# Optimization experiments

Measured on AMD Instinct MI355X. Metric: run time of the kernel, lower is better.

Reference implementation:

```python
import jax, jax.numpy as jnp
import numpy as np

N = 50000
E = 400000


def _cheb_norm(edge_index, dtype):
    # PyG ChebConv norm (normalization='sym', lambda_max=2.0):
    # remove self loops, L_hat = -D^{-1/2} A D^{-1/2} on off-diagonal edges.
    src, dst = edge_index[0], edge_index[1]
    mask = (src != dst).astype(dtype)
    deg = jax.ops.segment_sum(mask, src, num_segments=N)
    dinv = jnp.where(deg > 0, jax.lax.rsqrt(jnp.where(deg > 0, deg, 1.0)), 0.0)
    w = -dinv[src] * dinv[dst] * mask  # [E]
    return src, dst, w


def _cheb_conv(x, src, dst, w, W0, W1, b):
    # out = T0(x) W0 + T1(x) W1 + b, T0 = x, T1 = L_hat x
    tx1 = jax.ops.segment_sum(w[:, None] * x[src], dst, num_segments=N)
    return x @ W0 + tx1 @ W1 + b


def setup_inputs() -> dict:
    key = jax.random.key(0)
    ks = jax.random.split(key, 12)
    s = 0.05
    inp = {
        "x": jax.random.normal(ks[0], (N, 128), dtype=jnp.float32),
        "edge_index": jax.random.randint(ks[1], (2, E), 0, N, dtype=jnp.int64),
        "W1_0": jax.random.normal(ks[2], (128, 256), dtype=jnp.float32) * s,
        "W1_1": jax.random.normal(ks[3], (128, 256), dtype=jnp.float32) * s,
        "b1": jnp.zeros((256,), dtype=jnp.float32),
        "W2_0": jax.random.normal(ks[4], (256, 256), dtype=jnp.float32) * s,
        "W2_1": jax.random.normal(ks[5], (256, 256), dtype=jnp.float32) * s,
        "b2": jnp.zeros((256,), dtype=jnp.float32),
        "W3_0": jax.random.normal(ks[6], (256, 256), dtype=jnp.float32) * s,
        "W3_1": jax.random.normal(ks[7], (256, 256), dtype=jnp.float32) * s,
        "b3": jnp.zeros((256,), dtype=jnp.float32),
    }
    return inp


def reference(x, edge_index, W1_0, W1_1, b1, W2_0, W2_1, b2, W3_0, W3_1, b3):
    # Eval mode: F.dropout with training=False is identity, so dropout is omitted.
    src, dst, w = _cheb_norm(edge_index, x.dtype)
    h = jax.nn.relu(_cheb_conv(x, src, dst, w, W1_0, W1_1, b1))
    h = jax.nn.relu(_cheb_conv(h, src, dst, w, W2_0, W2_1, b2))
    h = _cheb_conv(h, src, dst, w, W3_0, W3_1, b3)
    return h
```

## Files before the change

kernel.cpp:

```cpp
#include <hip/hip_runtime.h>
#include <hip/hip_bf16.h>


typedef __attribute__((ext_vector_type(8))) short bf16x8;
typedef __attribute__((ext_vector_type(4))) float f32x4;

__device__ __forceinline__ float bf2f(unsigned int lo16) {
    unsigned int t = lo16 << 16;
    return __builtin_bit_cast(float, t);
}
__device__ __forceinline__ unsigned short f2bf(float f) {
    unsigned int u = __builtin_bit_cast(unsigned int, f);
    unsigned int r = (u + 0x7fffu + ((u >> 16) & 1u)) >> 16;
    return (unsigned short)r;
}

struct PrepParams {
    const int* src;
    const int* dst;
    float* deg;
    int* cnt;
    int E;
    const float* x;
    unsigned short* xb;
    int gE;
    int gC;
    const float* W[6];
    unsigned short* WT[6];
    int K[6];
};

__global__ __launch_bounds__(256) void prep_kernel(PrepParams p) {
    __shared__ float t[32][33];
    int b = blockIdx.x;
    int tid = threadIdx.x;
    if (b < p.gE) {
        int e = b * 256 + tid;
        if (e < p.E) {
            int s = p.src[e], d = p.dst[e];
            if (s != d) atomicAdd(&p.deg[s], 1.0f);
            atomicAdd(&p.cnt[d], 1);
        }
        return;
    }
    b -= p.gE;
    if (b < p.gC) {
        long long i = (long long)b * 256 + tid;
        float4 v = reinterpret_cast<const float4*>(p.x)[i];
        ushort4 o;
        o.x = f2bf(v.x); o.y = f2bf(v.y); o.z = f2bf(v.z); o.w = f2bf(v.w);
        reinterpret_cast<ushort4*>(p.xb)[i] = o;
        return;
    }
    b -= p.gC;
    int m = b >> 6;
    int rem = b & 63;
    int K = p.K[m];
    int kb = (rem & 7) * 32, nb = (rem >> 3) * 32;
    if (kb >= K) return;
    const float* W = p.W[m];
    unsigned short* WT = p.WT[m];
    int lx = tid & 31, ly = tid >> 5;
    #pragma unroll
    for (int i = 0; i < 32; i += 8)
        t[ly + i][lx] = W[(size_t)(kb + ly + i) * 256 + nb + lx];
    __syncthreads();
    #pragma unroll
    for (int i = 0; i < 32; i += 8)
        WT[(size_t)(nb + ly + i) * K + kb + lx] = f2bf(t[lx][ly + i]);
}

__global__ __launch_bounds__(256) void scan_partial_dinv(const int* __restrict__ cnt,
                                                         int* __restrict__ part,
                                                         float* __restrict__ deg, int N) {
    __shared__ int lds[256];
    int tid = threadIdx.x;
    int base = blockIdx.x * 1024 + tid * 4;
    int s = 0;
    #pragma unroll
    for (int i = 0; i < 4; ++i) {
        if (base + i < N) {
            s += cnt[base + i];
            float d = deg[base + i];
            deg[base + i] = (d > 0.0f) ? rsqrtf(d) : 0.0f;
        }
    }
    lds[tid] = s;
    __syncthreads();
    for (int off = 128; off > 0; off >>= 1) {
        if (tid < off) lds[tid] += lds[tid + off];
        __syncthreads();
    }
    if (tid == 0) part[blockIdx.x] = lds[0];
}

__global__ __launch_bounds__(64) void scan_small(int* __restrict__ part, int NB,
                                                 int* __restrict__ rowptr, int N) {
    int lane = threadIdx.x;
    int v = (lane < NB) ? part[lane] : 0;
    int inc = v;
    #pragma unroll
    for (int off = 1; off < 64; off <<= 1) {
        int t = __shfl_up(inc, off, 64);
        if (lane >= off) inc += t;
    }
    if (lane < NB) part[lane] = inc - v;
    if (lane == 63) rowptr[N] = inc;
}

__global__ __launch_bounds__(256) void scan_chunk(const int* __restrict__ cnt,
                                                  const int* __restrict__ part,
                                                  int* __restrict__ rowptr, int N) {
    __shared__ int lds[256];
    int tid = threadIdx.x;
    int base = blockIdx.x * 1024 + tid * 4;
    int c[4];
    #pragma unroll
    for (int i = 0; i < 4; ++i) c[i] = (base + i < N) ? cnt[base + i] : 0;
    int ts = c[0] + c[1] + c[2] + c[3];
    lds[tid] = ts;
    __syncthreads();
    for (int off = 1; off < 256; off <<= 1) {
        int v = (tid >= off) ? lds[tid - off] : 0;
        __syncthreads();
        lds[tid] += v;
        __syncthreads();
    }
    int o = part[blockIdx.x] + lds[tid] - ts;
    #pragma unroll
    for (int i = 0; i < 4; ++i) {
        if (base + i < N) rowptr[base + i] = o;
        o += c[i];
    }
}

__global__ __launch_bounds__(256) void fill_kernel(const int* __restrict__ src,
                                                   const int* __restrict__ dst,
                                                   const float* __restrict__ dinv,
                                                   const int* __restrict__ rowptr,
                                                   int* __restrict__ cnt2,
                                                   int* __restrict__ esrc,
                                                   float* __restrict__ ew, int E) {
    int e = blockIdx.x * blockDim.x + threadIdx.x;
    if (e < E) {
        int s = src[e], d = dst[e];
        int pos = rowptr[d] + atomicAdd(&cnt2[d], 1);
        esrc[pos] = s;
        ew[pos] = (s != d) ? (-dinv[s] * dinv[d]) : 0.0f;
    }
}

template <int V> struct RowT;
template <> struct RowT<4> { using T = uint2; };
template <> struct RowT<8> { using T = uint4; };

__device__ __forceinline__ void fma_row(float* acc, uint2 u, float wv) {
    acc[0] += wv * bf2f(u.x & 0xffffu);
    acc[1] += wv * bf2f(u.x >> 16);
    acc[2] += wv * bf2f(u.y & 0xffffu);
    acc[3] += wv * bf2f(u.y >> 16);
}
__device__ __forceinline__ void fma_row(float* acc, uint4 u, float wv) {
    acc[0] += wv * bf2f(u.x & 0xffffu);
    acc[1] += wv * bf2f(u.x >> 16);
    acc[2] += wv * bf2f(u.y & 0xffffu);
    acc[3] += wv * bf2f(u.y >> 16);
    acc[4] += wv * bf2f(u.z & 0xffffu);
    acc[5] += wv * bf2f(u.z >> 16);
    acc[6] += wv * bf2f(u.w & 0xffffu);
    acc[7] += wv * bf2f(u.w >> 16);
}
__device__ __forceinline__ void pack_out(unsigned short* q, const float* acc, uint2*) {
    uint2 o;
    o.x = (unsigned int)f2bf(acc[0]) | ((unsigned int)f2bf(acc[1]) << 16);
    o.y = (unsigned int)f2bf(acc[2]) | ((unsigned int)f2bf(acc[3]) << 16);
    *reinterpret_cast<uint2*>(q) = o;
}
__device__ __forceinline__ void pack_out(unsigned short* q, const float* acc, uint4*) {
    uint4 o;
    o.x = (unsigned int)f2bf(acc[0]) | ((unsigned int)f2bf(acc[1]) << 16);
    o.y = (unsigned int)f2bf(acc[2]) | ((unsigned int)f2bf(acc[3]) << 16);
    o.z = (unsigned int)f2bf(acc[4]) | ((unsigned int)f2bf(acc[5]) << 16);
    o.w = (unsigned int)f2bf(acc[6]) | ((unsigned int)f2bf(acc[7]) << 16);
    *reinterpret_cast<uint4*>(q) = o;
}

template <int F>
__global__ __launch_bounds__(256) void gather_bf16(const int* __restrict__ rowptr,
                                                   const int* __restrict__ esrc,
                                                   const float* __restrict__ ew,
                                                   const unsigned short* __restrict__ xb,
                                                   unsigned short* __restrict__ txb,
                                                   int N) {
    constexpr int V = F / 32;
    using T = typename RowT<V>::T;
    int half = threadIdx.x >> 5;
    int lane = threadIdx.x & 31;
    int n = blockIdx.x * 8 + half;
    if (n >= N) return;
    int beg = rowptr[n], end = rowptr[n + 1];
    float acc[V] = {};

    int k = beg;
    for (; k + 4 <= end; k += 4) {
        int s0 = esrc[k], s1 = esrc[k + 1], s2 = esrc[k + 2], s3 = esrc[k + 3];
        float w0 = ew[k], w1 = ew[k + 1], w2 = ew[k + 2], w3 = ew[k + 3];
        T r0 = *reinterpret_cast<const T*>(&xb[(size_t)s0 * F + lane * V]);
        T r1 = *reinterpret_cast<const T*>(&xb[(size_t)s1 * F + lane * V]);
        T r2 = *reinterpret_cast<const T*>(&xb[(size_t)s2 * F + lane * V]);
        T r3 = *reinterpret_cast<const T*>(&xb[(size_t)s3 * F + lane * V]);
        fma_row(acc, r0, w0);
        fma_row(acc, r1, w1);
        fma_row(acc, r2, w2);
        fma_row(acc, r3, w3);
    }
    for (; k < end; ++k) {
        int s = esrc[k];
        float wv = ew[k];
        T r = *reinterpret_cast<const T*>(&xb[(size_t)s * F + lane * V]);
        fma_row(acc, r, wv);
    }

    pack_out(&txb[(size_t)n * F + lane * V], acc, (T*)nullptr);
}

template <int K, bool RELU, typename OutT>
__global__ __launch_bounds__(256, 3) void gemm_mfma(const unsigned short* __restrict__ Xb,
                                                    const unsigned short* __restrict__ Tb,
                                                    const unsigned short* __restrict__ W0T,
                                                    const unsigned short* __restrict__ W1T,
                                                    const float* __restrict__ bias,
                                                    OutT* __restrict__ out, int M) {
    __shared__ unsigned short As[64 * 64];
    __shared__ unsigned short Bs[256 * 64];

    const int tid = threadIdx.x;
    const int wave = tid >> 6;
    const int lane = tid & 63;
    const int l15 = lane & 15;
    const int quad = lane >> 4;
    const int row0 = blockIdx.x * 64;
    const int swz = ((lane & 7) ^ ((lane >> 3) & 7)) * 8;

    f32x4 acc[4][4];
    #pragma unroll
    for (int i = 0; i < 4; ++i)
        #pragma unroll
        for (int j = 0; j < 4; ++j) acc[i][j] = (f32x4){0.f, 0.f, 0.f, 0.f};

    typedef const __attribute__((address_space(1))) void gvoid;
    typedef __attribute__((address_space(3))) void lvoid;

    #pragma unroll
    for (int pass = 0; pass < 2; ++pass) {
        const unsigned short* Amat = pass ? Tb : Xb;
        const unsigned short* Wmat = pass ? W1T : W0T;
        for (int k0 = 0; k0 < K; k0 += 64) {
            if (pass != 0 || k0 != 0) __syncthreads();
            #pragma unroll
            for (int r = 0; r < 2; ++r) {
                int grow = row0 + r * 32 + wave * 8 + (lane >> 3);
                if (grow > M - 1) grow = M - 1;
                const unsigned short* gp = &Amat[(size_t)grow * K + k0 + swz];
                __builtin_amdgcn_global_load_lds((gvoid*)gp,
                    (lvoid*)&As[(r * 32 + wave * 8) * 64], 16, 0, 0);
            }
            #pragma unroll
            for (int r = 0; r < 8; ++r) {
                int brow = r * 32 + wave * 8 + (lane >> 3);
                const unsigned short* gp = &Wmat[(size_t)brow * K + k0 + swz];
                __builtin_amdgcn_global_load_lds((gvoid*)gp,
                    (lvoid*)&Bs[(r * 32 + wave * 8) * 64], 16, 0, 0);
            }
            __syncthreads();

            #pragma unroll
            for (int kf = 0; kf < 2; ++kf) {
                const int col = (((kf * 4 + quad) ^ (l15 & 7)) * 8);
                bf16x8 a[4], b[4];
                #pragma unroll
                for (int mt = 0; mt < 4; ++mt)
                    a[mt] = *reinterpret_cast<const bf16x8*>(&As[(mt * 16 + l15) * 64 + col]);
                #pragma unroll
                for (int nt = 0; nt < 4; ++nt)
                    b[nt] = *reinterpret_cast<const bf16x8*>(
                        &Bs[(wave * 64 + nt * 16 + l15) * 64 + col]);
                #pragma unroll
                for (int mt = 0; mt < 4; ++mt)
                    #pragma unroll
                    for (int nt = 0; nt < 4; ++nt)
                        acc[mt][nt] = __builtin_amdgcn_mfma_f32_16x16x32_bf16(
                            a[mt], b[nt], acc[mt][nt], 0, 0, 0);
            }
        }
    }

    #pragma unroll
    for (int mt = 0; mt < 4; ++mt) {
        #pragma unroll
        for (int r = 0; r < 4; ++r) {
            int m = row0 + mt * 16 + quad * 4 + r;
            if (m >= M) continue;
            #pragma unroll
            for (int nt = 0; nt < 4; ++nt) {
                int n = wave * 64 + nt * 16 + l15;
                float v = acc[mt][nt][r] + bias[n];
                if (RELU) v = fmaxf(v, 0.0f);
                if constexpr (sizeof(OutT) == 2)
                    out[(size_t)m * 256 + n] = (OutT)f2bf(v);
                else
                    out[(size_t)m * 256 + n] = (OutT)v;
            }
        }
    }
}

static inline size_t align_up(size_t v, size_t a) { return (v + a - 1) / a * a; }

extern "C" void kernel_launch(void* const* d_in, const int* in_sizes, int n_in,
                              void* d_out, int out_size, void* d_ws, size_t ws_size,
                              hipStream_t stream) {
    const float* x    = (const float*)d_in[0];
    const int*   ei   = (const int*)d_in[1];
    const float* W1_0 = (const float*)d_in[2];
    const float* W1_1 = (const float*)d_in[3];
    const float* b1   = (const float*)d_in[4];
    const float* W2_0 = (const float*)d_in[5];
    const float* W2_1 = (const float*)d_in[6];
    const float* b2   = (const float*)d_in[7];
    const float* W3_0 = (const float*)d_in[8];
    const float* W3_1 = (const float*)d_in[9];
    const float* b3   = (const float*)d_in[10];
    float* out = (float*)d_out;

    const int N = in_sizes[0] / 128;
    const int E = in_sizes[1] / 2;
    const int* src = ei;
    const int* dst = ei + E;

    typedef unsigned short u16;
    char* ws = (char*)d_ws;
    size_t off = 0;
    float* dinv   = (float*)(ws + off); off = align_up(off + (size_t)N * 4, 256);
    int*   cnt    = (int*)  (ws + off); off = align_up(off + (size_t)N * 4, 256);
    int*   cnt2   = (int*)  (ws + off); off = align_up(off + (size_t)N * 4, 256);
    size_t zero_end = off;
    int*   rowptr = (int*)  (ws + off); off = align_up(off + (size_t)(N + 1) * 4, 256);
    int*   part   = (int*)  (ws + off); off = align_up(off + 256 * 4, 256);
    int*   esrc   = (int*)  (ws + off); off = align_up(off + (size_t)E * 4, 256);
    float* ew     = (float*)(ws + off); off = align_up(off + (size_t)E * 4, 256);
    u16*   xb     = (u16*)  (ws + off); off = align_up(off + (size_t)N * 128 * 2, 256);
    u16*   txb    = (u16*)  (ws + off); off = align_up(off + (size_t)N * 256 * 2, 256);
    u16*   h1b    = (u16*)  (ws + off); off = align_up(off + (size_t)N * 256 * 2, 256);
    u16*   h2b    = (u16*)  (ws + off); off = align_up(off + (size_t)N * 256 * 2, 256);
    u16*   W10T   = (u16*)  (ws + off); off = align_up(off + (size_t)256 * 128 * 2, 256);
    u16*   W11T   = (u16*)  (ws + off); off = align_up(off + (size_t)256 * 128 * 2, 256);
    u16*   W20T   = (u16*)  (ws + off); off = align_up(off + (size_t)256 * 256 * 2, 256);
    u16*   W21T   = (u16*)  (ws + off); off = align_up(off + (size_t)256 * 256 * 2, 256);
    u16*   W30T   = (u16*)  (ws + off); off = align_up(off + (size_t)256 * 256 * 2, 256);
    u16*   W31T   = (u16*)  (ws + off); off = align_up(off + (size_t)256 * 256 * 2, 256);
    (void)ws_size;

    const int TB = 256;
    const int gE = (E + TB - 1) / TB;
    const int gC = (int)(((long long)N * 128 / 4) / 256);
    const int NB = (N + 1023) / 1024;

    hipMemsetAsync(dinv, 0, zero_end, stream);

    {
        PrepParams p;
        p.src = src; p.dst = dst; p.deg = dinv; p.cnt = cnt; p.E = E;
        p.x = x; p.xb = xb; p.gE = gE; p.gC = gC;
        p.W[0] = W1_0; p.WT[0] = W10T; p.K[0] = 128;
        p.W[1] = W1_1; p.WT[1] = W11T; p.K[1] = 128;
        p.W[2] = W2_0; p.WT[2] = W20T; p.K[2] = 256;
        p.W[3] = W2_1; p.WT[3] = W21T; p.K[3] = 256;
        p.W[4] = W3_0; p.WT[4] = W30T; p.K[4] = 256;
        p.W[5] = W3_1; p.WT[5] = W31T; p.K[5] = 256;
        prep_kernel<<<gE + gC + 384, TB, 0, stream>>>(p);
    }

    scan_partial_dinv<<<NB, 256, 0, stream>>>(cnt, part, dinv, N);
    scan_small<<<1, 64, 0, stream>>>(part, NB, rowptr, N);
    scan_chunk<<<NB, 256, 0, stream>>>(cnt, part, rowptr, N);
    fill_kernel<<<(E + TB - 1) / TB, TB, 0, stream>>>(src, dst, dinv, rowptr, cnt2,
                                                      esrc, ew, E);

    dim3 gemmGrid((N + 63) / 64);
    dim3 gatherGrid((N + 7) / 8);

    gather_bf16<128><<<gatherGrid, TB, 0, stream>>>(rowptr, esrc, ew, xb, txb, N);
    gemm_mfma<128, true, u16><<<gemmGrid, TB, 0, stream>>>(xb, txb, W10T, W11T, b1, h1b, N);

    gather_bf16<256><<<gatherGrid, TB, 0, stream>>>(rowptr, esrc, ew, h1b, txb, N);
    gemm_mfma<256, true, u16><<<gemmGrid, TB, 0, stream>>>(h1b, txb, W20T, W21T, b2, h2b, N);

    gather_bf16<256><<<gatherGrid, TB, 0, stream>>>(rowptr, esrc, ew, h2b, txb, N);
    gemm_mfma<256, false, float><<<gemmGrid, TB, 0, stream>>>(h2b, txb, W30T, W31T, b3, out, N);
}
```

Before: 329.0 us.

## Build CSR with LDS-chunked histograms and shrink GEMM row tile to 32

Replaces the global-atomic degree/count and fill passes with per-chunk, per-range shared-memory histograms. Their counts are reduced and prefix-scanned into per-chunk bases, so the fill is deterministic and each edge takes an LDS atomic rank instead of a global atomic. The memset disappears because every histogram cell is written. Separately, the GEMM tile drops from 64 to 32 rows with occupancy hint 4, which doubles the grid but reuses the B tile less and reloads it twice as often.

```diff
diff --git a/kernel.cpp b/kernel.cpp
--- a/kernel.cpp
+++ b/kernel.cpp
@@ -4,6 +4,10 @@
 
 typedef __attribute__((ext_vector_type(8))) short bf16x8;
 typedef __attribute__((ext_vector_type(4))) float f32x4;
+
+#define NCH 16
+#define RBITS 13
+#define RBINS 8192
 
 __device__ __forceinline__ float bf2f(unsigned int lo16) {
     unsigned int t = lo16 << 16;
@@ -16,34 +20,18 @@
 }
 
 struct PrepParams {
-    const int* src;
-    const int* dst;
-    float* deg;
-    int* cnt;
-    int E;
     const float* x;
     unsigned short* xb;
-    int gE;
     int gC;
     const float* W[6];
     unsigned short* WT[6];
     int K[6];
 };
 
-__global__ __launch_bounds__(256) void prep_kernel(PrepParams p) {
+__global__ __launch_bounds__(256) void prep2_kernel(PrepParams p) {
     __shared__ float t[32][33];
     int b = blockIdx.x;
     int tid = threadIdx.x;
-    if (b < p.gE) {
-        int e = b * 256 + tid;
-        if (e < p.E) {
-            int s = p.src[e], d = p.dst[e];
-            if (s != d) atomicAdd(&p.deg[s], 1.0f);
-            atomicAdd(&p.cnt[d], 1);
-        }
-        return;
-    }
-    b -= p.gE;
     if (b < p.gC) {
         long long i = (long long)b * 256 + tid;
         float4 v = reinterpret_cast<const float4*>(p.x)[i];
@@ -70,19 +58,61 @@
         WT[(size_t)(nb + ly + i) * K + kb + lx] = f2bf(t[lx][ly + i]);
 }
 
-__global__ __launch_bounds__(256) void scan_partial_dinv(const int* __restrict__ cnt,
-                                                         int* __restrict__ part,
-                                                         float* __restrict__ deg, int N) {
+__global__ __launch_bounds__(256) void hist_kernel(const int* __restrict__ src,
+                                                   const int* __restrict__ dst,
+                                                   int* __restrict__ H,
+                                                   int* __restrict__ H2,
+                                                   int E, int NR, int NPAD) {
+    __shared__ int h[RBINS];
+    int tid = threadIdx.x;
+    int b = blockIdx.x;
+    int srcpass = (b >= NCH * NR);
+    if (srcpass) b -= NCH * NR;
+    int c = b / NR, r = b % NR;
+    int r0 = r << RBITS;
+    for (int i = tid; i < RBINS; i += 256) h[i] = 0;
+    __syncthreads();
+    int EC = (E + NCH - 1) / NCH;
+    int e0 = c * EC, e1 = min(e0 + EC, E);
+    if (!srcpass) {
+        for (int e = e0 + tid; e < e1; e += 256) {
+            int d = dst[e] - r0;
+            if ((unsigned)d < RBINS) atomicAdd(&h[d], 1);
+        }
+    } else {
+        for (int e = e0 + tid; e < e1; e += 256) {
+            int s = src[e];
+            int d = s - r0;
+            if ((unsigned)d < RBINS && s != dst[e]) atomicAdd(&h[d], 1);
+        }
+    }
+    __syncthreads();
+    int* out = (srcpass ? H2 : H) + (size_t)c * NPAD + r0;
+    for (int i = tid; i < RBINS; i += 256) out[i] = h[i];
+}
+
+__global__ __launch_bounds__(256) void reduce_scan_partial(const int* __restrict__ H,
+                                                           const int* __restrict__ H2,
+                                                           int* __restrict__ cnt,
+                                                           float* __restrict__ dinv,
+                                                           int* __restrict__ part,
+                                                           int N, int NPAD) {
     __shared__ int lds[256];
     int tid = threadIdx.x;
     int base = blockIdx.x * 1024 + tid * 4;
     int s = 0;
     #pragma unroll
     for (int i = 0; i < 4; ++i) {
-        if (base + i < N) {
-            s += cnt[base + i];
-            float d = deg[base + i];
-            deg[base + i] = (d > 0.0f) ? rsqrtf(d) : 0.0f;
+        int d = base + i;
+        if (d < N) {
+            int cn = 0, dg = 0;
+            for (int c = 0; c < NCH; ++c) {
+                cn += H[(size_t)c * NPAD + d];
+                dg += H2[(size_t)c * NPAD + d];
+            }
+            cnt[d] = cn;
+            dinv[d] = (dg > 0) ? rsqrtf((float)dg) : 0.0f;
+            s += cn;
         }
     }
     lds[tid] = s;
@@ -108,16 +138,19 @@
     if (lane == 63) rowptr[N] = inc;
 }
 
-__global__ __launch_bounds__(256) void scan_chunk(const int* __restrict__ cnt,
-                                                  const int* __restrict__ part,
-                                                  int* __restrict__ rowptr, int N) {
+__global__ __launch_bounds__(256) void scan_chunk_base(const int* __restrict__ cnt,
+                                                       const int* __restrict__ part,
+                                                       const int* __restrict__ H,
+                                                       int* __restrict__ rowptr,
+                                                       int* __restrict__ HS,
+                                                       int N, int NPAD) {
     __shared__ int lds[256];
     int tid = threadIdx.x;
     int base = blockIdx.x * 1024 + tid * 4;
-    int c[4];
-    #pragma unroll
-    for (int i = 0; i < 4; ++i) c[i] = (base + i < N) ? cnt[base + i] : 0;
-    int ts = c[0] + c[1] + c[2] + c[3];
+    int c4[4];
+    #pragma unroll
+    for (int i = 0; i < 4; ++i) c4[i] = (base + i < N) ? cnt[base + i] : 0;
+    int ts = c4[0] + c4[1] + c4[2] + c4[3];
     lds[tid] = ts;
     __syncthreads();
     for (int off = 1; off < 256; off <<= 1) {
@@ -129,24 +162,45 @@
     int o = part[blockIdx.x] + lds[tid] - ts;
     #pragma unroll
     for (int i = 0; i < 4; ++i) {
-        if (base + i < N) rowptr[base + i] = o;
-        o += c[i];
+        int d = base + i;
+        if (d < N) {
+            rowptr[d] = o;
+            int run = o;
+            for (int c = 0; c < NCH; ++c) {
+                HS[(size_t)c * NPAD + d] = run;
+                run += H[(size_t)c * NPAD + d];
+            }
+            o = run;
+        }
     }
 }
 
 __global__ __launch_bounds__(256) void fill_kernel(const int* __restrict__ src,
                                                    const int* __restrict__ dst,
                                                    const float* __restrict__ dinv,
-                                                   const int* __restrict__ rowptr,
-                                                   int* __restrict__ cnt2,
+                                                   const int* __restrict__ HS,
                                                    int* __restrict__ esrc,
-                                                   float* __restrict__ ew, int E) {
-    int e = blockIdx.x * blockDim.x + threadIdx.x;
-    if (e < E) {
-        int s = src[e], d = dst[e];
-        int pos = rowptr[d] + atomicAdd(&cnt2[d], 1);
-        esrc[pos] = s;
-        ew[pos] = (s != d) ? (-dinv[s] * dinv[d]) : 0.0f;
+                                                   float* __restrict__ ew,
+                                                   int E, int NR, int NPAD) {
+    __shared__ int h[RBINS];
+    int tid = threadIdx.x;
+    int b = blockIdx.x;
+    int c = b / NR, r = b % NR;
+    int r0 = r << RBITS;
+    for (int i = tid; i < RBINS; i += 256) h[i] = 0;
+    __syncthreads();
+    int EC = (E + NCH - 1) / NCH;
+    int e0 = c * EC, e1 = min(e0 + EC, E);
+    for (int e = e0 + tid; e < e1; e += 256) {
+        int d = dst[e];
+        int dl = d - r0;
+        if ((unsigned)dl < RBINS) {
+            int s = src[e];
+            int rank = atomicAdd(&h[dl], 1);
+            int pos = HS[(size_t)c * NPAD + d] + rank;
+            esrc[pos] = s;
+            ew[pos] = (s != d) ? (-dinv[s] * dinv[d]) : 0.0f;
+        }
     }
 }
 
@@ -225,13 +279,13 @@
 }
 
 template <int K, bool RELU, typename OutT>
-__global__ __launch_bounds__(256, 3) void gemm_mfma(const unsigned short* __restrict__ Xb,
+__global__ __launch_bounds__(256, 4) void gemm_mfma(const unsigned short* __restrict__ Xb,
                                                     const unsigned short* __restrict__ Tb,
                                                     const unsigned short* __restrict__ W0T,
                                                     const unsigned short* __restrict__ W1T,
                                                     const float* __restrict__ bias,
                                                     OutT* __restrict__ out, int M) {
-    __shared__ unsigned short As[64 * 64];
+    __shared__ unsigned short As[32 * 64];
     __shared__ unsigned short Bs[256 * 64];
 
     const int tid = threadIdx.x;
@@ -239,12 +293,12 @@
     const int lane = tid & 63;
     const int l15 = lane & 15;
     const int quad = lane >> 4;
-    const int row0 = blockIdx.x * 64;
+    const int row0 = blockIdx.x * 32;
     const int swz = ((lane & 7) ^ ((lane >> 3) & 7)) * 8;
 
-    f32x4 acc[4][4];
-    #pragma unroll
-    for (int i = 0; i < 4; ++i)
+    f32x4 acc[2][4];
+    #pragma unroll
+    for (int i = 0; i < 2; ++i)
         #pragma unroll
         for (int j = 0; j < 4; ++j) acc[i][j] = (f32x4){0.f, 0.f, 0.f, 0.f};
 
@@ -257,13 +311,12 @@
         const unsigned short* Wmat = pass ? W1T : W0T;
         for (int k0 = 0; k0 < K; k0 += 64) {
             if (pass != 0 || k0 != 0) __syncthreads();
-            #pragma unroll
-            for (int r = 0; r < 2; ++r) {
-                int grow = row0 + r * 32 + wave * 8 + (lane >> 3);
+            {
+                int grow = row0 + wave * 8 + (lane >> 3);
                 if (grow > M - 1) grow = M - 1;
                 const unsigned short* gp = &Amat[(size_t)grow * K + k0 + swz];
                 __builtin_amdgcn_global_load_lds((gvoid*)gp,
-                    (lvoid*)&As[(r * 32 + wave * 8) * 64], 16, 0, 0);
+                    (lvoid*)&As[(wave * 8) * 64], 16, 0, 0);
             }
             #pragma unroll
             for (int r = 0; r < 8; ++r) {
@@ -277,16 +330,16 @@
             #pragma unroll
             for (int kf = 0; kf < 2; ++kf) {
                 const int col = (((kf * 4 + quad) ^ (l15 & 7)) * 8);
-                bf16x8 a[4], b[4];
+                bf16x8 a[2], b[4];
                 #pragma unroll
-                for (int mt = 0; mt < 4; ++mt)
+                for (int mt = 0; mt < 2; ++mt)
                     a[mt] = *reinterpret_cast<const bf16x8*>(&As[(mt * 16 + l15) * 64 + col]);
                 #pragma unroll
                 for (int nt = 0; nt < 4; ++nt)
                     b[nt] = *reinterpret_cast<const bf16x8*>(
                         &Bs[(wave * 64 + nt * 16 + l15) * 64 + col]);
                 #pragma unroll
-                for (int mt = 0; mt < 4; ++mt)
+                for (int mt = 0; mt < 2; ++mt)
                     #pragma unroll
                     for (int nt = 0; nt < 4; ++nt)
                         acc[mt][nt] = __builtin_amdgcn_mfma_f32_16x16x32_bf16(
@@ -296,7 +349,7 @@
     }
 
     #pragma unroll
-    for (int mt = 0; mt < 4; ++mt) {
+    for (int mt = 0; mt < 2; ++mt) {
         #pragma unroll
         for (int r = 0; r < 4; ++r) {
             int m = row0 + mt * 16 + quad * 4 + r;
@@ -338,15 +391,19 @@
     const int* src = ei;
     const int* dst = ei + E;
 
+    const int NR = (N + RBINS - 1) / RBINS;
+    const int NPAD = NR * RBINS;
+
     typedef unsigned short u16;
     char* ws = (char*)d_ws;
     size_t off = 0;
     float* dinv   = (float*)(ws + off); off = align_up(off + (size_t)N * 4, 256);
     int*   cnt    = (int*)  (ws + off); off = align_up(off + (size_t)N * 4, 256);
-    int*   cnt2   = (int*)  (ws + off); off = align_up(off + (size_t)N * 4, 256);
-    size_t zero_end = off;
     int*   rowptr = (int*)  (ws + off); off = align_up(off + (size_t)(N + 1) * 4, 256);
     int*   part   = (int*)  (ws + off); off = align_up(off + 256 * 4, 256);
+    int*   H      = (int*)  (ws + off); off = align_up(off + (size_t)NCH * NPAD * 4, 256);
+    int*   H2     = (int*)  (ws + off); off = align_up(off + (size_t)NCH * NPAD * 4, 256);
+    int*   HS     = (int*)  (ws + off); off = align_up(off + (size_t)NCH * NPAD * 4, 256);
     int*   esrc   = (int*)  (ws + off); off = align_up(off + (size_t)E * 4, 256);
     float* ew     = (float*)(ws + off); off = align_up(off + (size_t)E * 4, 256);
     u16*   xb     = (u16*)  (ws + off); off = align_up(off + (size_t)N * 128 * 2, 256);
@@ -362,32 +419,28 @@
     (void)ws_size;
 
     const int TB = 256;
-    const int gE = (E + TB - 1) / TB;
     const int gC = (int)(((long long)N * 128 / 4) / 256);
     const int NB = (N + 1023) / 1024;
 
-    hipMemsetAsync(dinv, 0, zero_end, stream);
-
     {
         PrepParams p;
-        p.src = src; p.dst = dst; p.deg = dinv; p.cnt = cnt; p.E = E;
-        p.x = x; p.xb = xb; p.gE = gE; p.gC = gC;
+        p.x = x; p.xb = xb; p.gC = gC;
         p.W[0] = W1_0; p.WT[0] = W10T; p.K[0] = 128;
         p.W[1] = W1_1; p.WT[1] = W11T; p.K[1] = 128;
         p.W[2] = W2_0; p.WT[2] = W20T; p.K[2] = 256;
         p.W[3] = W2_1; p.WT[3] = W21T; p.K[3] = 256;
         p.W[4] = W3_0; p.WT[4] = W30T; p.K[4] = 256;
         p.W[5] = W3_1; p.WT[5] = W31T; p.K[5] = 256;
-        prep_kernel<<<gE + gC + 384, TB, 0, stream>>>(p);
-    }
-
-    scan_partial_dinv<<<NB, 256, 0, stream>>>(cnt, part, dinv, N);
+        prep2_kernel<<<gC + 384, TB, 0, stream>>>(p);
+    }
+
+    hist_kernel<<<2 * NCH * NR, TB, 0, stream>>>(src, dst, H, H2, E, NR, NPAD);
+    reduce_scan_partial<<<NB, TB, 0, stream>>>(H, H2, cnt, dinv, part, N, NPAD);
     scan_small<<<1, 64, 0, stream>>>(part, NB, rowptr, N);
-    scan_chunk<<<NB, 256, 0, stream>>>(cnt, part, rowptr, N);
-    fill_kernel<<<(E + TB - 1) / TB, TB, 0, stream>>>(src, dst, dinv, rowptr, cnt2,
-                                                      esrc, ew, E);
-
-    dim3 gemmGrid((N + 63) / 64);
+    scan_chunk_base<<<NB, TB, 0, stream>>>(cnt, part, H, rowptr, HS, N, NPAD);
+    fill_kernel<<<NCH * NR, TB, 0, stream>>>(src, dst, dinv, HS, esrc, ew, E, NR, NPAD);
+
+    dim3 gemmGrid((N + 31) / 32);
     dim3 gatherGrid((N + 7) / 8);
 
     gather_bf16<128><<<gatherGrid, TB, 0, stream>>>(rowptr, esrc, ew, xb, txb, N);
```

New measurement: 396.6 us. +20.6%, slower.
